# Kernel optimization log

Hardware: AMD Instinct MI355X
Metric: run time of the kernel (lower is better)

## Reference

```python
import jax, jax.numpy as jnp
import numpy as np

# ---- hyperparameters (from args defaults) ----
TEMPERATURE = 0.07
ALPHA = 0.5
OT_EPSILON = 0.1
OT_ITERS = 20
HOLO_WEIGHT = 1.0
RKD_DISTANCE_WEIGHT = 1.0
RKD_ANGLE_WEIGHT = 2.0
GLOBAL_RKD_WEIGHT = 10.0
MATRYOSHKA_DIMS = [128, 768]
MATRYOSHKA_WEIGHTS = [1.0, 2.0]

B, N, H_S, H_T, D_REP = 64, 256, 768, 1024, 768


def l2norm(x, axis=-1):
    # F.normalize(p=2): x / max(||x||, eps)
    n = jnp.sqrt(jnp.sum(x * x, axis=axis, keepdims=True))
    return x / jnp.maximum(n, 1e-12)


def pairwise_distance(x):
    # [n, d] -> [n, n] squared-euclidean-style distances
    sq = jnp.sum(x * x, axis=1, keepdims=True)
    return sq + sq.T - 2.0 * (x @ x.T)


def huber(diff):
    a = jnp.abs(diff)
    return jnp.where(a < 1.0, 0.5 * a * a, a - 0.5)


def rkd_distance_loss(s, t):
    n = s.shape[0]
    mask = jnp.triu(jnp.ones((n, n), dtype=bool), k=1)
    cnt = jnp.sum(mask.astype(s.dtype))
    ds, dt = pairwise_distance(s), pairwise_distance(t)
    mean_s = jax.lax.stop_gradient(jnp.sum(jnp.where(mask, ds, 0.0)) / cnt) + 1e-8
    mean_t = jax.lax.stop_gradient(jnp.sum(jnp.where(mask, dt, 0.0)) / cnt) + 1e-8
    loss = huber(ds / mean_s - dt / mean_t)
    return jnp.sum(jnp.where(mask, loss, 0.0)) / cnt


def angle_potentials(x):
    # diffs[i, j] = x[j] - x[i]
    diffs = x[None, :, :] - x[:, None, :]
    e = diffs / (jnp.linalg.norm(diffs, axis=-1, keepdims=True) + 1e-8)
    return jnp.einsum('ijd,kjd->ijk', e, e)


def rkd_angle_loss(s, t):
    psi_s, psi_t = angle_potentials(s), angle_potentials(t)
    n = psi_s.shape[0]
    idx = jnp.arange(n)
    i, j, k = idx[:, None, None], idx[None, :, None], idx[None, None, :]
    mask = (i != j) & (i != k) & (j != k)  # exclude degenerate triplets
    cnt = jnp.sum(mask.astype(s.dtype))
    loss = huber(psi_s - psi_t)
    return jnp.sum(jnp.where(mask, loss, 0.0)) / cnt


def saliency_measure(h, temp=1.0):
    # softmax over token axis of hidden-state norms -> [B, N, 1]
    norms = jnp.linalg.norm(h, axis=-1)
    return jax.nn.softmax(norms / temp, axis=-1)[..., None]


def structure_matrix(z):
    zn = l2norm(z, axis=-1)
    return 1.0 - jnp.einsum('bnd,bmd->bnm', zn, zn)


def sinkhorn_knopp_log_domain(C, mu, nu):
    # C: [B, Ns, Nt]; mu: [B, Ns, 1]; nu: [B, Nt, 1]
    log_K = -C / OT_EPSILON
    log_mu = jnp.log(mu + 1e-8)
    log_nu = jnp.log(nu + 1e-8)
    u = jnp.zeros_like(mu)
    v = jnp.zeros_like(nu)
    for _ in range(OT_ITERS):
        u = log_mu - jax.scipy.special.logsumexp(
            log_K + jnp.swapaxes(v, 1, 2), axis=2, keepdims=True)
        v = log_nu - jax.scipy.special.logsumexp(
            jnp.swapaxes(log_K, 1, 2) + jnp.swapaxes(u, 1, 2),
            axis=2, keepdims=True)
    return jnp.exp(u + log_K + jnp.swapaxes(v, 1, 2))


def fused_gromov_wasserstein(z_s, z_t, proj_w, proj_b):
    mu = saliency_measure(z_s)   # [B, N, 1]
    nu = saliency_measure(z_t)   # [B, N, 1]
    C_s = structure_matrix(z_s)  # [B, N, N]
    C_t = structure_matrix(z_t)
    z_s_norm = l2norm(z_s @ proj_w + proj_b, axis=-1)
    z_t_norm = l2norm(z_t, axis=-1)
    M = 1.0 - jnp.einsum('bnd,bmd->bnm', z_s_norm, z_t_norm)
    Gamma = sinkhorn_knopp_log_domain(M, mu, nu)
    feat_loss = jnp.mean(jnp.sum(M * Gamma, axis=(1, 2)))
    Gamma_norm = Gamma / (jnp.sum(Gamma, axis=2, keepdims=True) + 1e-8)
    C_t_mapped = jnp.einsum('bnm,bmk,blk->bnl', Gamma_norm, C_t, Gamma_norm)
    w = jnp.einsum('bni,bmi->bnm', mu, mu)  # mu @ mu^T
    struct_loss = jnp.mean(jnp.sum((C_s - C_t_mapped) ** 2 * w, axis=(1, 2)))
    return (1.0 - ALPHA) * feat_loss + ALPHA * struct_loss


def cross_entropy_inbatch(scores):
    # labels = arange(B)
    logZ = jax.scipy.special.logsumexp(scores, axis=1)
    return jnp.mean(logZ - jnp.diagonal(scores))


def setup_inputs() -> dict:
    key = jax.random.key(0)
    ks = jax.random.split(key, 10)
    return {
        's_q_reps': jax.random.normal(ks[0], (B, D_REP), jnp.float32),
        's_p_reps': jax.random.normal(ks[1], (B, D_REP), jnp.float32),
        't_q_reps': jax.random.normal(ks[2], (B, D_REP), jnp.float32),
        't_p_reps': jax.random.normal(ks[3], (B, D_REP), jnp.float32),
        's_q_states': jax.random.normal(ks[4], (B, N, H_S), jnp.float32),
        's_p_states': jax.random.normal(ks[5], (B, N, H_S), jnp.float32),
        't_q_states': jax.random.normal(ks[6], (B, N, H_T), jnp.float32),
        't_p_states': jax.random.normal(ks[7], (B, N, H_T), jnp.float32),
        'proj_w': jax.random.normal(ks[8], (H_S, H_T), jnp.float32) * (H_S ** -0.5),
        'proj_b': jnp.zeros((H_T,), jnp.float32),
    }


def reference(s_q_reps, s_p_reps, t_q_reps, t_p_reps,
              s_q_states, s_p_states, t_q_states, t_p_states,
              proj_w, proj_b):
    # teacher outputs are computed under torch.no_grad()
    t_q_reps = jax.lax.stop_gradient(t_q_reps)
    t_p_reps = jax.lax.stop_gradient(t_p_reps)
    t_q_states = jax.lax.stop_gradient(t_q_states)
    t_p_states = jax.lax.stop_gradient(t_p_states)

    contrastive_acc = 0.0
    holo_acc = 0.0
    rkd_acc = 0.0
    for dim, dim_weight in zip(MATRYOSHKA_DIMS, MATRYOSHKA_WEIGHTS):
        s_q_slice = l2norm(s_q_reps[:, :dim])
        s_p_slice = l2norm(s_p_reps[:, :dim])
        scores = (s_q_slice @ s_p_slice.T) / TEMPERATURE
        contrastive_acc += dim_weight * cross_entropy_inbatch(scores)
        if dim <= 128:
            s_batch = jnp.concatenate([s_q_slice, s_p_slice], axis=0)
            t_batch = jnp.concatenate(
                [l2norm(t_q_reps[:, :dim]), l2norm(t_p_reps[:, :dim])], axis=0)
            loss_dist = rkd_distance_loss(s_batch, t_batch)
            loss_angle = rkd_angle_loss(s_batch, t_batch)
            rkd_val = (RKD_DISTANCE_WEIGHT * loss_dist
                       + RKD_ANGLE_WEIGHT * loss_angle)
            rkd_acc += GLOBAL_RKD_WEIGHT * rkd_val * 2.0
        else:
            loss_q = fused_gromov_wasserstein(s_q_states, t_q_states, proj_w, proj_b)
            loss_p = fused_gromov_wasserstein(s_p_states, t_p_states, proj_w, proj_b)
            holo_acc += HOLO_WEIGHT * 0.5 * (loss_q + loss_p)
    return contrastive_acc + holo_acc + rkd_acc
```

## Files before the change

### kernel.cpp

```cpp
#include <hip/hip_runtime.h>
#include <math.h>

#define NB   64
#define NN   256
#define HSS  768
#define HTT  1024
#define ROWS (NB*NN)
#define C2LOG 14.426950408889634f

typedef unsigned short u16;
typedef __attribute__((ext_vector_type(8))) short bf16x8;
typedef __attribute__((ext_vector_type(4))) float f32x4;

#define LIDX(r,c) (((r)<<8) + (((((c)>>3) + (r)) & 31)<<3) + ((c)&7))
#define EIDX(r,c) (((r)<<7) + (((((c)>>3) + (r)) & 15)<<3) + ((c)&7))

__device__ __forceinline__ void gl16(const u16* g, u16* l){
  __builtin_amdgcn_global_load_lds(
      (const __attribute__((address_space(1))) unsigned int*)g,
      (__attribute__((address_space(3))) unsigned int*)l,
      16, 0, 0);
}

static const size_t OFF_ACC   = 0;
static const size_t OFF_SQ128 = 16;
static const size_t OFF_SP128 = OFF_SQ128 + 64*128;
static const size_t OFF_TQ128 = OFF_SP128 + 64*128;
static const size_t OFF_TP128 = OFF_TQ128 + 64*128;
static const size_t OFF_SQ768 = OFF_TP128 + 64*128;
static const size_t OFF_SP768 = OFF_SQ768 + 64*768;
static const size_t OFF_DS    = OFF_SP768 + 64*768;
static const size_t OFF_DT    = OFF_DS + 128*128;
static const size_t OFF_CS    = OFF_DT + 128*128;
static const size_t OFF_MBF   = OFF_CS  + (size_t)2*NB*NN*NN;
static const size_t OFF_ZS_BF = OFF_MBF + (size_t)NB*NN*NN;
static const size_t OFF_ZT_BF = OFF_ZS_BF + (size_t)ROWS*HSS/2;
static const size_t OFF_WT_BF = OFF_ZT_BF + (size_t)ROWS*HTT/2;
static const size_t OFF_ZSP_BF= OFF_WT_BF + (size_t)HTT*HSS/2;
static const size_t OFF_GN_BF = OFF_ZSP_BF+ (size_t)ROWS*HTT/2;
static const size_t OFF_CT_BF = OFF_GN_BF + (size_t)NB*NN*NN;
static const size_t OFF_T_BF  = OFF_ZS_BF;
static const size_t OFF_NS    = OFF_CT_BF + (size_t)NB*NN*NN;
static const size_t OFF_NT    = OFF_NS + ROWS;
static const size_t OFF_NSP   = OFF_NT + ROWS;
static const size_t OFF_MU    = OFF_NSP + ROWS;
static const size_t OFF_NU    = OFF_MU + 2*ROWS;


__device__ __forceinline__ float wred_sum(float v){
  #pragma unroll
  for(int o=32;o>0;o>>=1) v += __shfl_xor(v,o,64);
  return v;
}
__device__ __forceinline__ float wred_max(float v){
  #pragma unroll
  for(int o=32;o>0;o>>=1) v = fmaxf(v, __shfl_xor(v,o,64));
  return v;
}
__device__ __forceinline__ u16 f2bf(float f){
  unsigned u = __float_as_uint(f);
  unsigned r = (u + 0x7fffu + ((u>>16)&1u)) >> 16;
  return (u16)r;
}
__device__ __forceinline__ float bf2f(u16 h){
  return __uint_as_float(((unsigned)h)<<16);
}

__global__ __launch_bounds__(256) void k_l2norm_all(
    const float* __restrict__ sq, const float* __restrict__ sp,
    const float* __restrict__ tq, const float* __restrict__ tp,
    float* __restrict__ ws){
  int bid = blockIdx.x;
  int r = bid & 63;
  const float* in; float* out; int kuse;
  if(bid < 64)       { in = sq; out = ws + OFF_SQ128; kuse = 128; }
  else if(bid < 128) { in = sp; out = ws + OFF_SP128; kuse = 128; }
  else if(bid < 192) { in = tq; out = ws + OFF_TQ128; kuse = 128; }
  else if(bid < 256) { in = tp; out = ws + OFF_TP128; kuse = 128; }
  else if(bid < 320) { in = sq; out = ws + OFF_SQ768; kuse = 768; }
  else               { in = sp; out = ws + OFF_SP768; kuse = 768; }
  const float* row = in + (size_t)r*768;
  float ss = 0.f;
  for(int d=threadIdx.x; d<kuse; d+=256){ float x=row[d]; ss += x*x; }
  ss = wred_sum(ss);
  __shared__ float sm[4];
  if((threadIdx.x&63)==0) sm[threadIdx.x>>6]=ss;
  __syncthreads();
  float tot = sm[0]+sm[1]+sm[2]+sm[3];
  float inv = 1.f / fmaxf(sqrtf(tot), 1e-12f);
  for(int d=threadIdx.x; d<kuse; d+=256) out[(size_t)r*kuse + d] = row[d]*inv;
}

__global__ __launch_bounds__(512) void k_contrastive2(const float* __restrict__ ws,
    float* __restrict__ acc){
  int bid = blockIdx.x;
  int i = bid & 63;
  int big = bid >> 6;
  const float* q = ws + (big ? OFF_SQ768 : OFF_SQ128);
  const float* p = ws + (big ? OFF_SP768 : OFF_SP128);
  int dim = big ? 768 : 128;
  float weight = big ? 2.f : 1.f;
  int j = threadIdx.x & 63;
  int part = threadIdx.x >> 6;
  const float* qi = q + (size_t)i*dim;
  const float* pj = p + (size_t)j*dim;
  int seg = dim >> 3;
  int d0 = part*seg;
  float dot = 0.f;
  for(int d=d0; d<d0+seg; d+=4){
    float4 a = *(const float4*)(qi+d);
    float4 b = *(const float4*)(pj+d);
    dot = fmaf(a.x,b.x,dot);
    dot = fmaf(a.y,b.y,dot);
    dot = fmaf(a.z,b.z,dot);
    dot = fmaf(a.w,b.w,dot);
  }
  __shared__ float sm[8][64];
  sm[part][j] = dot;
  __syncthreads();
  if(part==0){
    float s = 0.f;
    #pragma unroll
    for(int k=0;k<8;k++) s += sm[k][j];
    s = s / 0.07f;
    float mx = wred_max(s);
    float e = expf(s - mx);
    float Z = wred_sum(e);
    float logZ = mx + logf(Z);
    float diag = __shfl(s, i, 64);
    if(j==0) atomicAdd(acc+0, weight*(logZ - diag)*(1.f/64.f));
  }
}

__global__ __launch_bounds__(128) void k_gram_ds(const float* __restrict__ sb,
    const float* __restrict__ tb, float* __restrict__ ds, float* __restrict__ dt,
    float* __restrict__ acc){
  int r = blockIdx.x, c = threadIdx.x;
  const float* sr = sb + r*128; const float* sc = sb + c*128;
  const float* tr = tb + r*128; const float* tc = tb + c*128;
  float dot_s=0,ssr=0,ssc=0,dot_t=0,tsr=0,tsc=0;
  for(int d=0; d<128; d++){
    float a=sr[d], b=sc[d]; dot_s += a*b; ssr += a*a; ssc += b*b;
    float at=tr[d], bt=tc[d]; dot_t += at*bt; tsr += at*at; tsc += bt*bt;
  }
  float dv = ssr + ssc - 2.f*dot_s;
  float tv = tsr + tsc - 2.f*dot_t;
  ds[r*128+c] = dv; dt[r*128+c] = tv;
  float ms = (c>r)? dv : 0.f;
  float mt = (c>r)? tv : 0.f;
  ms = wred_sum(ms); mt = wred_sum(mt);
  __shared__ float sm[2][2];
  if((threadIdx.x&63)==0){ sm[0][threadIdx.x>>6]=ms; sm[1][threadIdx.x>>6]=mt; }
  __syncthreads();
  if(threadIdx.x==0){ atomicAdd(acc+1, sm[0][0]+sm[0][1]); atomicAdd(acc+2, sm[1][0]+sm[1][1]); }
}

__global__ __launch_bounds__(128) void k_rkd_dist(const float* __restrict__ ds,
    const float* __restrict__ dt, float* __restrict__ acc){
  int r=blockIdx.x, c=threadIdx.x;
  float mean_s = acc[1]*(1.f/8128.f) + 1e-8f;
  float mean_t = acc[2]*(1.f/8128.f) + 1e-8f;
  float h=0.f;
  if(c>r){
    float diff = ds[r*128+c]/mean_s - dt[r*128+c]/mean_t;
    float a = fabsf(diff);
    h = (a<1.f)? 0.5f*a*a : a-0.5f;
  }
  h = wred_sum(h);
  __shared__ float sm[2];
  if((threadIdx.x&63)==0) sm[threadIdx.x>>6]=h;
  __syncthreads();
  if(threadIdx.x==0) atomicAdd(acc+3, sm[0]+sm[1]);
}

#define RKD_LDS 65536
__global__ __launch_bounds__(256, 1) void k_rkd_angle_mfma(
    const float* __restrict__ sb, const float* __restrict__ tb,
    float* __restrict__ accp)
{
  extern __shared__ u16 eSh[];
  u16* Es = eSh;
  u16* Et = eSh + 128*128;
  const int j    = blockIdx.x >> 1;
  const int half = blockIdx.x & 1;
  const int tid = threadIdx.x;
  {
    const int i = tid >> 1, h = tid & 1;
    #pragma unroll
    for(int which=0; which<2; which++){
      const float* xb = which ? tb : sb;
      u16* E = which ? Et : Es;
      const float* xj = xb + j*128 + h*64;
      const float* xi = xb + i*128 + h*64;
      float ss = 0.f;
      #pragma unroll
      for(int d4=0; d4<16; d4++){
        float4 a = *(const float4*)(xj + d4*4);
        float4 b = *(const float4*)(xi + d4*4);
        float d0=a.x-b.x, d1=a.y-b.y, d2=a.z-b.z, d3=a.w-b.w;
        ss += d0*d0+d1*d1+d2*d2+d3*d3;
      }
      ss += __shfl_xor(ss, 1, 64);
      float inv = (i==j) ? 0.f : 1.f/(sqrtf(ss)+1e-8f);
      #pragma unroll
      for(int d4=0; d4<16; d4++){
        float4 a = *(const float4*)(xj + d4*4);
        float4 b = *(const float4*)(xi + d4*4);
        int c = h*64 + d4*4;
        E[EIDX(i,c+0)] = f2bf((a.x-b.x)*inv);
        E[EIDX(i,c+1)] = f2bf((a.y-b.y)*inv);
        E[EIDX(i,c+2)] = f2bf((a.z-b.z)*inv);
        E[EIDX(i,c+3)] = f2bf((a.w-b.w)*inv);
      }
    }
  }
  __syncthreads();
  const int w = tid >> 6, lane = tid & 63;
  const int q = lane >> 4, loc = lane & 15;
  float hsum = 0.f;
  #pragma unroll
  for(int ni=0; ni<4; ni++){
    const int cb = half*64 + ni*16;
    #pragma unroll
    for(int mi=0; mi<2; mi++){
      const int rb = w*32 + mi*16;
      f32x4 as_ = {0.f,0.f,0.f,0.f}, at_ = {0.f,0.f,0.f,0.f};
      #pragma unroll
      for(int k0=0; k0<128; k0+=32){
        int ra = rb + loc, rbn = cb + loc;
        int ca = k0 + q*8;
        bf16x8 aS = *(const bf16x8*)(Es + EIDX(ra, ca));
        bf16x8 bS = *(const bf16x8*)(Es + EIDX(rbn, ca));
        bf16x8 aT = *(const bf16x8*)(Et + EIDX(ra, ca));
        bf16x8 bT = *(const bf16x8*)(Et + EIDX(rbn, ca));
        as_ = __builtin_amdgcn_mfma_f32_16x16x32_bf16(aS, bS, as_, 0,0,0);
        at_ = __builtin_amdgcn_mfma_f32_16x16x32_bf16(aT, bT, at_, 0,0,0);
      }
      #pragma unroll
      for(int jj=0; jj<4; jj++){
        int row = rb + q*4 + jj, col = cb + loc;
        if(row != col){
          float d = as_[jj] - at_[jj];
          float a = fabsf(d);
          hsum += (a < 1.f) ? 0.5f*a*a : a - 0.5f;
        }
      }
    }
  }
  hsum = wred_sum(hsum);
  __syncthreads();
  float* red = (float*)eSh;
  if(lane==0) red[w] = hsum;
  __syncthreads();
  if(tid==0) atomicAdd(accp+4, red[0]+red[1]+red[2]+red[3]);
}

__global__ __launch_bounds__(256) void k_cvt_norm(const float* __restrict__ in,
    u16* __restrict__ out, float* __restrict__ nrm, int K){
  int w = threadIdx.x >> 6, l = threadIdx.x & 63;
  int r = blockIdx.x*4 + w;
  const float* row = in + (size_t)r*K;
  u16* orow = out + (size_t)r*K;
  float ss = 0.f;
  int nv = K >> 8;
  for(int i=0;i<nv;i++){
    int d = l*4 + i*256;
    float4 x = *(const float4*)(row + d);
    ushort4 o; o.x=f2bf(x.x); o.y=f2bf(x.y); o.z=f2bf(x.z); o.w=f2bf(x.w);
    *(ushort4*)(orow + d) = o;
    ss += x.x*x.x + x.y*x.y + x.z*x.z + x.w*x.w;
  }
  ss = wred_sum(ss);
  if(l==0) nrm[r] = sqrtf(ss);
}

__global__ __launch_bounds__(256) void k_row_norm_bf16(const u16* __restrict__ z,
    float* __restrict__ nrm, int K){
  int w = threadIdx.x >> 6, l = threadIdx.x & 63;
  int r = blockIdx.x*4 + w;
  const u16* row = z + (size_t)r*K;
  float ss = 0.f;
  int nv = K >> 9;
  for(int i=0;i<nv;i++){
    int d = l*8 + i*512;
    uint4 v = *(const uint4*)(row + d);
    float a0=__uint_as_float(v.x<<16), a1=__uint_as_float(v.x&0xffff0000u);
    float a2=__uint_as_float(v.y<<16), a3=__uint_as_float(v.y&0xffff0000u);
    float a4=__uint_as_float(v.z<<16), a5=__uint_as_float(v.z&0xffff0000u);
    float a6=__uint_as_float(v.w<<16), a7=__uint_as_float(v.w&0xffff0000u);
    ss += a0*a0+a1*a1+a2*a2+a3*a3+a4*a4+a5*a5+a6*a6+a7*a7;
  }
  ss = wred_sum(ss);
  if(l==0) nrm[r] = sqrtf(ss);
}

__global__ void k_wt(const float* __restrict__ W, u16* __restrict__ Wt){
  __shared__ float t[32][33];
  int k0 = blockIdx.y*32, n0 = blockIdx.x*32;
  int tx = threadIdx.x, ty = threadIdx.y;
  for(int r=0;r<32;r+=8) t[ty+r][tx] = W[(size_t)(k0+ty+r)*HTT + n0+tx];
  __syncthreads();
  for(int r=0;r<32;r+=8) Wt[(size_t)(n0+ty+r)*HSS + k0+tx] = f2bf(t[tx][ty+r]);
}

__global__ __launch_bounds__(256) void k_saliency2(const float* __restrict__ ns,
    const float* __restrict__ nt, float* __restrict__ omu, float* __restrict__ onu){
  int b0 = blockIdx.x, n = threadIdx.x;
  const float* nrm = (b0 < NB) ? ns : nt;
  float* out = (b0 < NB) ? omu : onu;
  int b = b0 & 63;
  float x = nrm[b*NN+n];
  float mx = wred_max(x);
  __shared__ float sm[4], sm2[4];
  if((n&63)==0) sm[n>>6]=mx;
  __syncthreads();
  mx = fmaxf(fmaxf(sm[0],sm[1]),fmaxf(sm[2],sm[3]));
  float e = expf(x-mx);
  float s = wred_sum(e);
  if((n&63)==0) sm2[n>>6]=s;
  __syncthreads();
  s = sm2[0]+sm2[1]+sm2[2]+sm2[3];
  out[b*NN+n] = e/s;
}

enum { MODE_PROJ=0, MODE_COST=1, MODE_PLAIN=2, MODE_STRUCT=3 };

template<int MODE>
__global__ __launch_bounds__(256) void k_mfma(
    const u16* __restrict__ A, int lda, long bA,
    const u16* __restrict__ B, int ldb, long bB,
    int K,
    float* __restrict__ outF, u16* __restrict__ outB, int ldo, long bO,
    const float* __restrict__ nx, const float* __restrict__ ny,
    const float* __restrict__ bias,
    const float* __restrict__ Cs, const float* __restrict__ mu,
    float* __restrict__ accp)
{
  __shared__ u16 As[128*32];
  __shared__ u16 Bs[128*32];
  __shared__ float red[4];

  int gx = gridDim.x, gy = gridDim.y;
  int flat = blockIdx.x + gx*(blockIdx.y + gy*blockIdx.z);
  int nwg  = gx*gy*gridDim.z;
  int cpx  = nwg >> 3;
  int lg   = (flat & 7)*cpx + (flat >> 3);
  int bx   = lg % gx;
  int rest = lg / gx;
  int by   = rest % gy;
  int b    = rest / gy;

  const u16* Ab = A + (size_t)b*bA;
  const u16* Bb = B + (size_t)b*bB;
  int tid = threadIdx.x;
  int lane = tid & 63, w = tid >> 6;
  int m0 = by*128, n0 = bx*128;
  int row_off = (w>>1)*64, col_off = (w&1)*64;
  int q = lane>>4, loc = lane&15;
  f32x4 acc[4][4] = {};

  const int srow = (lane >> 2);
  const int sslot = lane & 3;

  for(int k0=0;k0<K;k0+=32){
    #pragma unroll
    for(int h=0;h<2;h++){
      int row = h*64 + w*16 + srow;
      int ca  = (sslot ^ ((row>>1)&3))*8;
      u16* ldst = As + h*2048 + w*512 + lane*8;
      u16* ldstB= Bs + h*2048 + w*512 + lane*8;
      gl16(Ab + (size_t)(m0+row)*lda + k0 + ca, ldst);
      gl16(Bb + (size_t)(n0+row)*ldb + k0 + ca, ldstB);
    }
    __syncthreads();
    bf16x8 af[4], bfr[4];
    #pragma unroll
    for(int mi=0;mi<4;mi++){
      int r = row_off + mi*16 + loc;
      int slot = q ^ ((r>>1)&3);
      af[mi] = *(const bf16x8*)(As + r*32 + slot*8);
    }
    #pragma unroll
    for(int ni=0;ni<4;ni++){
      int r = col_off + ni*16 + loc;
      int slot = q ^ ((r>>1)&3);
      bfr[ni] = *(const bf16x8*)(Bs + r*32 + slot*8);
    }
    #pragma unroll
    for(int mi=0;mi<4;mi++)
      #pragma unroll
      for(int ni=0;ni<4;ni++)
        acc[mi][ni] = __builtin_amdgcn_mfma_f32_16x16x32_bf16(af[mi], bfr[ni], acc[mi][ni], 0,0,0);
    __syncthreads();
  }

  float* outFb = outF ? outF + (size_t)b*bO : nullptr;
  u16*   outBb = outB ? outB + (size_t)b*bO : nullptr;
  const float* nxb = nx ? nx + (size_t)b*NN : nullptr;
  const float* nyb = ny ? ny + (size_t)b*NN : nullptr;
  const float* Cb  = (MODE==MODE_STRUCT) ? Cs + (size_t)b*bO : nullptr;
  const float* mb  = (MODE==MODE_STRUCT) ? mu + (size_t)b*NN : nullptr;
  float lsum = 0.f;
  #pragma unroll
  for(int mi=0;mi<4;mi++){
    #pragma unroll
    for(int j=0;j<4;j++){
      int row = m0 + row_off + mi*16 + q*4 + j;
      float ir = 0.f, mr = 0.f;
      if(MODE==MODE_COST)   ir = 1.f/fmaxf(nxb[row],1e-12f);
      if(MODE==MODE_STRUCT) mr = mb[row];
      #pragma unroll
      for(int ni=0;ni<4;ni++){
        int col = n0 + col_off + ni*16 + loc;
        float v = acc[mi][ni][j];
        if(MODE==MODE_PROJ){
          v += bias[col];
          outBb[(size_t)row*ldo + col] = f2bf(v);
        } else if(MODE==MODE_COST){
          float ic = 1.f/fmaxf(nyb[col],1e-12f);
          v = 1.f - v*ir*ic;
          if(outFb) outFb[(size_t)row*ldo + col] = v;
          if(outBb) outBb[(size_t)row*ldo + col] = f2bf(v);
        } else if(MODE==MODE_PLAIN){
          outBb[(size_t)row*ldo + col] = f2bf(v);
        } else {
          float d = Cb[(size_t)row*ldo + col] - v;
          lsum += d*d*mr*mb[col];
        }
      }
    }
  }
  if(MODE==MODE_STRUCT){
    lsum = wred_sum(lsum);
    if(lane==0) red[w] = lsum;
    __syncthreads();
    if(tid==0) atomicAdd(accp+6, red[0]+red[1]+red[2]+red[3]);
  }
}

#define SINK_DYN_LDS 131072
__global__ __launch_bounds__(1024, 1) void k_sinkhorn_fused(
    const u16* __restrict__ Mbf, const float* __restrict__ muL,
    const float* __restrict__ nuL, u16* __restrict__ Gn, float* __restrict__ accp)
{
  extern __shared__ u16 Ks[];
  __shared__ __align__(16) float part[4096];
  __shared__ __align__(16) float su[NN], sv[NN], smu[NN], snu[NN];
  __shared__ float red[16];

  const int b = blockIdx.x;
  const int t = threadIdx.x;
  const u16* Mb = Mbf + (size_t)b*NN*NN;

  #pragma unroll
  for(int i=0;i<16;i++){
    int e = (i*1024 + t)*4;
    int r = e>>8, c = e&255;
    ushort4 mv = *(const ushort4*)(Mb + e);
    ushort4 o;
    o.x = f2bf(exp2f(-C2LOG*bf2f(mv.x)));
    o.y = f2bf(exp2f(-C2LOG*bf2f(mv.y)));
    o.z = f2bf(exp2f(-C2LOG*bf2f(mv.z)));
    o.w = f2bf(exp2f(-C2LOG*bf2f(mv.w)));
    *(ushort4*)(Ks + LIDX(r,c)) = o;
  }
  if(t < NN){
    smu[t] = muL[(size_t)b*NN+t] + 1e-8f;
    snu[t] = nuL[(size_t)b*NN+t] + 1e-8f;
    sv[t] = 1.f;
  }
  __syncthreads();

  const int r_ = t & 255, p_ = t >> 8;
  const int w = t>>6, l = t&63;

  for(int it=0; it<20; it++){
    {
      float s0=0.f, s1=0.f, s2=0.f, s3=0.f;
      #pragma unroll
      for(int jj=0;jj<8;jj++){
        int c0 = p_*64 + jj*8;
        uint4 kv = *(const uint4*)(Ks + LIDX(r_, c0));
        float4 va = *(const float4*)(sv + c0);
        float4 vb = *(const float4*)(sv + c0 + 4);
        s0 = fmaf(__uint_as_float(kv.x<<16),           va.x, s0);
        s1 = fmaf(__uint_as_float(kv.x & 0xffff0000u), va.y, s1);
        s2 = fmaf(__uint_as_float(kv.y<<16),           va.z, s2);
        s3 = fmaf(__uint_as_float(kv.y & 0xffff0000u), va.w, s3);
        s0 = fmaf(__uint_as_float(kv.z<<16),           vb.x, s0);
        s1 = fmaf(__uint_as_float(kv.z & 0xffff0000u), vb.y, s1);
        s2 = fmaf(__uint_as_float(kv.w<<16),           vb.z, s2);
        s3 = fmaf(__uint_as_float(kv.w & 0xffff0000u), vb.w, s3);
      }
      part[t] = (s0+s1)+(s2+s3);
    }
    __syncthreads();
    if(t < NN){
      float S = part[t] + part[256+t] + part[512+t] + part[768+t];
      su[t] = smu[t] / S;
    }
    __syncthreads();
    {
      float cs0=0.f,cs1=0.f,cs2=0.f,cs3=0.f;
      #pragma unroll
      for(int rr=0;rr<16;rr++){
        int r = w*16 + rr;
        ushort4 kv = *(const ushort4*)(Ks + LIDX(r, l*4));
        float ur = su[r];
        cs0 = fmaf(bf2f(kv.x), ur, cs0);
        cs1 = fmaf(bf2f(kv.y), ur, cs1);
        cs2 = fmaf(bf2f(kv.z), ur, cs2);
        cs3 = fmaf(bf2f(kv.w), ur, cs3);
      }
      float4 o; o.x=cs0; o.y=cs1; o.z=cs2; o.w=cs3;
      *(float4*)(part + w*256 + l*4) = o;
    }
    __syncthreads();
    if(t < NN){
      float S = 0.f;
      #pragma unroll
      for(int ww=0;ww<16;ww++) S += part[ww*256 + t];
      sv[t] = snu[t] / S;
    }
    __syncthreads();
  }

  {
    float s0=0.f, s1=0.f, s2=0.f, s3=0.f;
    #pragma unroll
    for(int jj=0;jj<8;jj++){
      int c0 = p_*64 + jj*8;
      uint4 kv = *(const uint4*)(Ks + LIDX(r_, c0));
      float4 va = *(const float4*)(sv + c0);
      float4 vb = *(const float4*)(sv + c0 + 4);
      s0 = fmaf(__uint_as_float(kv.x<<16),           va.x, s0);
      s1 = fmaf(__uint_as_float(kv.x & 0xffff0000u), va.y, s1);
      s2 = fmaf(__uint_as_float(kv.y<<16),           va.z, s2);
      s3 = fmaf(__uint_as_float(kv.y & 0xffff0000u), va.w, s3);
      s0 = fmaf(__uint_as_float(kv.z<<16),           vb.x, s0);
      s1 = fmaf(__uint_as_float(kv.z & 0xffff0000u), vb.y, s1);
      s2 = fmaf(__uint_as_float(kv.w<<16),           vb.z, s2);
      s3 = fmaf(__uint_as_float(kv.w & 0xffff0000u), vb.w, s3);
    }
    part[t] = (s0+s1)+(s2+s3);
  }
  __syncthreads();
  if(t < NN){
    float S = part[t] + part[256+t] + part[512+t] + part[768+t];
    smu[t] = 1.f / (su[t]*S + 1e-8f);
  }
  __syncthreads();

  u16* Gb = Gn + (size_t)b*NN*NN;
  const float IC = -1.f/C2LOG;
  float v0 = sv[l*4+0], v1 = sv[l*4+1], v2 = sv[l*4+2], v3 = sv[l*4+3];
  float fl = 0.f;
  for(int rr=0;rr<16;rr++){
    int r = w*16 + rr;
    ushort4 kv = *(const ushort4*)(Ks + LIDX(r, l*4));
    float k0=bf2f(kv.x), k1=bf2f(kv.y), k2=bf2f(kv.z), k3=bf2f(kv.w);
    float ur = su[r], inv = smu[r];
    float g0=ur*k0*v0, g1=ur*k1*v1, g2=ur*k2*v2, g3=ur*k3*v3;
    fl += g0*(__log2f(k0)*IC) + g1*(__log2f(k1)*IC)
        + g2*(__log2f(k2)*IC) + g3*(__log2f(k3)*IC);
    ushort4 o;
    o.x=f2bf(g0*inv); o.y=f2bf(g1*inv); o.z=f2bf(g2*inv); o.w=f2bf(g3*inv);
    *(ushort4*)(Gb + (size_t)r*NN + l*4) = o;
  }
  fl = wred_sum(fl);
  if(l==0) red[w] = fl;
  __syncthreads();
  if(t==0){
    float s=0.f;
    #pragma unroll
    for(int i=0;i<16;i++) s+=red[i];
    atomicAdd(accp+5, s);
  }
}

__global__ void k_final(const float* __restrict__ acc, float* __restrict__ out){
  out[0] = acc[0]
         + 20.f*acc[3]*(1.f/8128.f)
         + 40.f*acc[4]*(1.f/2048256.f)
         + 0.25f*(acc[5]+acc[6])*(1.f/64.f);
}

extern "C" void kernel_launch(void* const* d_in, const int* in_sizes, int n_in,
                              void* d_out, int out_size, void* d_ws, size_t ws_size,
                              hipStream_t stream) {
  const float* s_q_reps   = (const float*)d_in[0];
  const float* s_p_reps   = (const float*)d_in[1];
  const float* t_q_reps   = (const float*)d_in[2];
  const float* t_p_reps   = (const float*)d_in[3];
  const float* s_q_states = (const float*)d_in[4];
  const float* s_p_states = (const float*)d_in[5];
  const float* t_q_states = (const float*)d_in[6];
  const float* t_p_states = (const float*)d_in[7];
  const float* proj_w     = (const float*)d_in[8];
  const float* proj_b     = (const float*)d_in[9];
  float* ws = (float*)d_ws;
  float* acc = ws + OFF_ACC;
  u16* M_BF   = (u16*)(ws + OFF_MBF);
  u16* ZS_BF  = (u16*)(ws + OFF_ZS_BF);
  u16* ZT_BF  = (u16*)(ws + OFF_ZT_BF);
  u16* WT_BF  = (u16*)(ws + OFF_WT_BF);
  u16* ZSP_BF = (u16*)(ws + OFF_ZSP_BF);
  u16* GN_BF  = (u16*)(ws + OFF_GN_BF);
  u16* CT_BF  = (u16*)(ws + OFF_CT_BF);
  u16* T_BF   = (u16*)(ws + OFF_T_BF);

  hipFuncSetAttribute(reinterpret_cast<const void*>(k_sinkhorn_fused),
                      hipFuncAttributeMaxDynamicSharedMemorySize, SINK_DYN_LDS);
  hipFuncSetAttribute(reinterpret_cast<const void*>(k_rkd_angle_mfma),
                      hipFuncAttributeMaxDynamicSharedMemorySize, RKD_LDS);

  hipMemsetAsync(acc, 0, 16*sizeof(float), stream);

  k_l2norm_all<<<384,256,0,stream>>>(s_q_reps, s_p_reps, t_q_reps, t_p_reps, ws);
  k_contrastive2<<<128,512,0,stream>>>(ws, acc);
  k_gram_ds<<<128,128,0,stream>>>(ws+OFF_SQ128, ws+OFF_TQ128, ws+OFF_DS, ws+OFF_DT, acc);
  k_rkd_dist<<<128,128,0,stream>>>(ws+OFF_DS, ws+OFF_DT, acc);
  k_rkd_angle_mfma<<<256,256,RKD_LDS,stream>>>(ws+OFF_SQ128, ws+OFF_TQ128, acc);

  k_wt<<<dim3(HTT/32, HSS/32),dim3(32,8),0,stream>>>(proj_w, WT_BF);

  for(int pass=0; pass<2; pass++){
    const float* zs = pass ? s_p_states : s_q_states;
    const float* zt = pass ? t_p_states : t_q_states;
    size_t po  = (size_t)pass*NB*NN*NN;
    size_t pr  = (size_t)pass*ROWS;
    k_cvt_norm<<<ROWS/4,256,0,stream>>>(zs, ZS_BF, ws+OFF_NS, HSS);
    k_cvt_norm<<<ROWS/4,256,0,stream>>>(zt, ZT_BF, ws+OFF_NT, HTT);
    k_saliency2<<<128,256,0,stream>>>(ws+OFF_NS, ws+OFF_NT, ws+OFF_MU+pr, ws+OFF_NU+pr);
    k_mfma<MODE_PROJ><<<dim3(HTT/128, ROWS/128, 1),256,0,stream>>>(
        ZS_BF, HSS, 0, WT_BF, HSS, 0, HSS,
        nullptr, ZSP_BF, HTT, 0,
        nullptr, nullptr, proj_b, nullptr, nullptr, nullptr);
    k_row_norm_bf16<<<ROWS/4,256,0,stream>>>(ZSP_BF, ws+OFF_NSP, HTT);
    k_mfma<MODE_COST><<<dim3(2,2,NB),256,0,stream>>>(
        ZS_BF, HSS, (long)NN*HSS, ZS_BF, HSS, (long)NN*HSS, HSS,
        ws+OFF_CS+po, nullptr, NN, (long)NN*NN,
        ws+OFF_NS, ws+OFF_NS, nullptr, nullptr, nullptr, nullptr);
    k_mfma<MODE_COST><<<dim3(2,2,NB),256,0,stream>>>(
        ZT_BF, HTT, (long)NN*HTT, ZT_BF, HTT, (long)NN*HTT, HTT,
        nullptr, CT_BF+po, NN, (long)NN*NN,
        ws+OFF_NT, ws+OFF_NT, nullptr, nullptr, nullptr, nullptr);
    k_mfma<MODE_COST><<<dim3(2,2,NB),256,0,stream>>>(
        ZSP_BF, HTT, (long)NN*HTT, ZT_BF, HTT, (long)NN*HTT, HTT,
        nullptr, M_BF+po, NN, (long)NN*NN,
        ws+OFF_NSP, ws+OFF_NT, nullptr, nullptr, nullptr, nullptr);
  }

  k_sinkhorn_fused<<<2*NB,1024,SINK_DYN_LDS,stream>>>(
      M_BF, ws+OFF_MU, ws+OFF_NU, GN_BF, acc);

  k_mfma<MODE_PLAIN><<<dim3(2,2,2*NB),256,0,stream>>>(
      GN_BF, NN, (long)NN*NN, CT_BF, NN, (long)NN*NN, NN,
      nullptr, T_BF, NN, (long)NN*NN,
      nullptr, nullptr, nullptr, nullptr, nullptr, nullptr);
  k_mfma<MODE_STRUCT><<<dim3(2,2,2*NB),256,0,stream>>>(
      T_BF, NN, (long)NN*NN, GN_BF, NN, (long)NN*NN, NN,
      nullptr, nullptr, NN, (long)NN*NN,
      nullptr, nullptr, nullptr, ws+OFF_CS, ws+OFF_MU, acc);

  k_final<<<1,1,0,stream>>>(acc, (float*)d_out);
}
```

Baseline: 671.5 us.

## Merge small prep kernels and use 64x64 MFMA tiles for batched cost GEMMs

Fuses the bf16 conversion and norm kernels for both state tensors with the RKD gram computation into one launch, and merges the RKD distance reduction with the pass-0 saliency softmax into another. Adds a 64x64-tile MFMA GEMM variant with XCD-aware block remapping and uses it for the per-batch 256x256 cost, plain and structure GEMMs. This raises block count from 256 to 1024+ per launch to fill more CUs. The trade-off is less reuse per tile and a single-buffered K loop with two barriers per step.

```diff
diff --git a/kernel.cpp b/kernel.cpp
--- a/kernel.cpp
+++ b/kernel.cpp
@@ -132,45 +132,106 @@
   }
 }
 
-__global__ __launch_bounds__(128) void k_gram_ds(const float* __restrict__ sb,
-    const float* __restrict__ tb, float* __restrict__ ds, float* __restrict__ dt,
-    float* __restrict__ acc){
-  int r = blockIdx.x, c = threadIdx.x;
-  const float* sr = sb + r*128; const float* sc = sb + c*128;
-  const float* tr = tb + r*128; const float* tc = tb + c*128;
-  float dot_s=0,ssr=0,ssc=0,dot_t=0,tsr=0,tsc=0;
-  for(int d=0; d<128; d++){
-    float a=sr[d], b=sc[d]; dot_s += a*b; ssr += a*a; ssc += b*b;
-    float at=tr[d], bt=tc[d]; dot_t += at*bt; tsr += at*at; tsc += bt*bt;
-  }
-  float dv = ssr + ssc - 2.f*dot_s;
-  float tv = tsr + tsc - 2.f*dot_t;
-  ds[r*128+c] = dv; dt[r*128+c] = tv;
-  float ms = (c>r)? dv : 0.f;
-  float mt = (c>r)? tv : 0.f;
-  ms = wred_sum(ms); mt = wred_sum(mt);
+__global__ __launch_bounds__(256) void k_pack_cvt(
+    const float* __restrict__ zs, const float* __restrict__ zt,
+    u16* __restrict__ zsb, u16* __restrict__ ztb,
+    float* __restrict__ ns, float* __restrict__ nt,
+    const float* __restrict__ sb128, const float* __restrict__ tb128,
+    float* __restrict__ ds, float* __restrict__ dt, float* __restrict__ acc)
+{
   __shared__ float sm[2][2];
-  if((threadIdx.x&63)==0){ sm[0][threadIdx.x>>6]=ms; sm[1][threadIdx.x>>6]=mt; }
-  __syncthreads();
-  if(threadIdx.x==0){ atomicAdd(acc+1, sm[0][0]+sm[0][1]); atomicAdd(acc+2, sm[1][0]+sm[1][1]); }
-}
-
-__global__ __launch_bounds__(128) void k_rkd_dist(const float* __restrict__ ds,
-    const float* __restrict__ dt, float* __restrict__ acc){
-  int r=blockIdx.x, c=threadIdx.x;
-  float mean_s = acc[1]*(1.f/8128.f) + 1e-8f;
-  float mean_t = acc[2]*(1.f/8128.f) + 1e-8f;
-  float h=0.f;
-  if(c>r){
-    float diff = ds[r*128+c]/mean_s - dt[r*128+c]/mean_t;
-    float a = fabsf(diff);
-    h = (a<1.f)? 0.5f*a*a : a-0.5f;
-  }
-  h = wred_sum(h);
-  __shared__ float sm[2];
-  if((threadIdx.x&63)==0) sm[threadIdx.x>>6]=h;
-  __syncthreads();
-  if(threadIdx.x==0) atomicAdd(acc+3, sm[0]+sm[1]);
+  int bid = blockIdx.x;
+  if(bid < 8192){
+    const float* in; u16* out; float* nrm; int K; int cb;
+    if(bid < 4096){ in=zs; out=zsb; nrm=ns; K=HSS; cb=bid; }
+    else          { in=zt; out=ztb; nrm=nt; K=HTT; cb=bid-4096; }
+    int w = threadIdx.x >> 6, l = threadIdx.x & 63;
+    int r = cb*4 + w;
+    const float* row = in + (size_t)r*K;
+    u16* orow = out + (size_t)r*K;
+    float ss = 0.f;
+    int nv = K >> 8;
+    for(int i=0;i<nv;i++){
+      int d = l*4 + i*256;
+      float4 x = *(const float4*)(row + d);
+      ushort4 o; o.x=f2bf(x.x); o.y=f2bf(x.y); o.z=f2bf(x.z); o.w=f2bf(x.w);
+      *(ushort4*)(orow + d) = o;
+      ss += x.x*x.x + x.y*x.y + x.z*x.z + x.w*x.w;
+    }
+    ss = wred_sum(ss);
+    if(l==0) nrm[r] = sqrtf(ss);
+    return;
+  }
+  {
+    int r = bid - 8192;
+    int c = threadIdx.x;
+    float ms = 0.f, mt = 0.f;
+    if(c < 128){
+      const float* sr = sb128 + r*128; const float* sc = sb128 + c*128;
+      const float* tr = tb128 + r*128; const float* tc = tb128 + c*128;
+      float dot_s=0,ssr=0,ssc=0,dot_t=0,tsr=0,tsc=0;
+      for(int d=0; d<128; d++){
+        float a=sr[d], bb=sc[d]; dot_s += a*bb; ssr += a*a; ssc += bb*bb;
+        float at=tr[d], bt=tc[d]; dot_t += at*bt; tsr += at*at; tsc += bt*bt;
+      }
+      float dv = ssr + ssc - 2.f*dot_s;
+      float tv = tsr + tsc - 2.f*dot_t;
+      ds[r*128+c] = dv; dt[r*128+c] = tv;
+      ms = (c>r)? dv : 0.f;
+      mt = (c>r)? tv : 0.f;
+      ms = wred_sum(ms); mt = wred_sum(mt);
+      if((c&63)==0){ sm[0][c>>6]=ms; sm[1][c>>6]=mt; }
+    }
+    __syncthreads();
+    if(threadIdx.x==0){
+      atomicAdd(acc+1, sm[0][0]+sm[0][1]);
+      atomicAdd(acc+2, sm[1][0]+sm[1][1]);
+    }
+  }
+}
+
+__global__ __launch_bounds__(256) void k_small0(
+    const float* __restrict__ ds, const float* __restrict__ dt,
+    const float* __restrict__ ns, const float* __restrict__ nt,
+    float* __restrict__ omu, float* __restrict__ onu, float* __restrict__ acc)
+{
+  __shared__ float sm[4], sm2[4];
+  int bid = blockIdx.x;
+  if(bid < 128){
+    int r = bid, c = threadIdx.x;
+    float mean_s = acc[1]*(1.f/8128.f) + 1e-8f;
+    float mean_t = acc[2]*(1.f/8128.f) + 1e-8f;
+    float h = 0.f;
+    if(c < 128){
+      if(c > r){
+        float diff = ds[r*128+c]/mean_s - dt[r*128+c]/mean_t;
+        float a = fabsf(diff);
+        h = (a<1.f)? 0.5f*a*a : a-0.5f;
+      }
+      h = wred_sum(h);
+      if((c&63)==0) sm[c>>6]=h;
+    }
+    __syncthreads();
+    if(threadIdx.x==0) atomicAdd(acc+3, sm[0]+sm[1]);
+    return;
+  }
+  {
+    int b0 = bid - 128, n = threadIdx.x;
+    const float* nrm = (b0 < NB) ? ns : nt;
+    float* out = (b0 < NB) ? omu : onu;
+    int b = b0 & 63;
+    float x = nrm[b*NN+n];
+    float mx = wred_max(x);
+    if((n&63)==0) sm[n>>6]=mx;
+    __syncthreads();
+    mx = fmaxf(fmaxf(sm[0],sm[1]),fmaxf(sm[2],sm[3]));
+    float e = expf(x-mx);
+    float s = wred_sum(e);
+    if((n&63)==0) sm2[n>>6]=s;
+    __syncthreads();
+    s = sm2[0]+sm2[1]+sm2[2]+sm2[3];
+    out[b*NN+n] = e/s;
+  }
 }
 
 #define RKD_LDS 65536
@@ -253,25 +314,6 @@
   if(lane==0) red[w] = hsum;
   __syncthreads();
   if(tid==0) atomicAdd(accp+4, red[0]+red[1]+red[2]+red[3]);
-}
-
-__global__ __launch_bounds__(256) void k_cvt_norm(const float* __restrict__ in,
-    u16* __restrict__ out, float* __restrict__ nrm, int K){
-  int w = threadIdx.x >> 6, l = threadIdx.x & 63;
-  int r = blockIdx.x*4 + w;
-  const float* row = in + (size_t)r*K;
-  u16* orow = out + (size_t)r*K;
-  float ss = 0.f;
-  int nv = K >> 8;
-  for(int i=0;i<nv;i++){
-    int d = l*4 + i*256;
-    float4 x = *(const float4*)(row + d);
-    ushort4 o; o.x=f2bf(x.x); o.y=f2bf(x.y); o.z=f2bf(x.z); o.w=f2bf(x.w);
-    *(ushort4*)(orow + d) = o;
-    ss += x.x*x.x + x.y*x.y + x.z*x.z + x.w*x.w;
-  }
-  ss = wred_sum(ss);
-  if(l==0) nrm[r] = sqrtf(ss);
 }
 
 __global__ __launch_bounds__(256) void k_row_norm_bf16(const u16* __restrict__ z,
@@ -411,6 +453,118 @@
       if(MODE==MODE_STRUCT) mr = mb[row];
       #pragma unroll
       for(int ni=0;ni<4;ni++){
+        int col = n0 + col_off + ni*16 + loc;
+        float v = acc[mi][ni][j];
+        if(MODE==MODE_PROJ){
+          v += bias[col];
+          outBb[(size_t)row*ldo + col] = f2bf(v);
+        } else if(MODE==MODE_COST){
+          float ic = 1.f/fmaxf(nyb[col],1e-12f);
+          v = 1.f - v*ir*ic;
+          if(outFb) outFb[(size_t)row*ldo + col] = v;
+          if(outBb) outBb[(size_t)row*ldo + col] = f2bf(v);
+        } else if(MODE==MODE_PLAIN){
+          outBb[(size_t)row*ldo + col] = f2bf(v);
+        } else {
+          float d = Cb[(size_t)row*ldo + col] - v;
+          lsum += d*d*mr*mb[col];
+        }
+      }
+    }
+  }
+  if(MODE==MODE_STRUCT){
+    lsum = wred_sum(lsum);
+    if(lane==0) red[w] = lsum;
+    __syncthreads();
+    if(tid==0) atomicAdd(accp+6, red[0]+red[1]+red[2]+red[3]);
+  }
+}
+
+template<int MODE>
+__global__ __launch_bounds__(256) void k_mfma64(
+    const u16* __restrict__ A, int lda, long bA,
+    const u16* __restrict__ B, int ldb, long bB,
+    int K,
+    float* __restrict__ outF, u16* __restrict__ outB, int ldo, long bO,
+    const float* __restrict__ nx, const float* __restrict__ ny,
+    const float* __restrict__ bias,
+    const float* __restrict__ Cs, const float* __restrict__ mu,
+    float* __restrict__ accp)
+{
+  __shared__ u16 As[64*32];
+  __shared__ u16 Bs[64*32];
+  __shared__ float red[4];
+
+  int gx = gridDim.x, gy = gridDim.y;
+  int flat = blockIdx.x + gx*(blockIdx.y + gy*blockIdx.z);
+  int nwg  = gx*gy*gridDim.z;
+  int cpx  = nwg >> 3;
+  int lg   = (flat & 7)*cpx + (flat >> 3);
+  int bx   = lg % gx;
+  int rest = lg / gx;
+  int by   = rest % gy;
+  int b    = rest / gy;
+
+  const u16* Ab = A + (size_t)b*bA;
+  const u16* Bb = B + (size_t)b*bB;
+  int tid = threadIdx.x;
+  int lane = tid & 63, w = tid >> 6;
+  int m0 = by*64, n0 = bx*64;
+  int row_off = (w>>1)*32, col_off = (w&1)*32;
+  int q = lane>>4, loc = lane&15;
+  f32x4 acc[2][2] = {};
+
+  const int srow = tid >> 2;
+  const int sslot = tid & 3;
+
+  for(int k0=0;k0<K;k0+=32){
+    {
+      int row = srow;
+      int ca  = (sslot ^ ((row>>1)&3))*8;
+      u16* la = As + w*512 + lane*8;
+      u16* lb = Bs + w*512 + lane*8;
+      gl16(Ab + (size_t)(m0+row)*lda + k0 + ca, la);
+      gl16(Bb + (size_t)(n0+row)*ldb + k0 + ca, lb);
+    }
+    __syncthreads();
+    bf16x8 af[2], bfr[2];
+    #pragma unroll
+    for(int mi=0;mi<2;mi++){
+      int r = row_off + mi*16 + loc;
+      int slot = q ^ ((r>>1)&3);
+      af[mi] = *(const bf16x8*)(As + r*32 + slot*8);
+    }
+    #pragma unroll
+    for(int ni=0;ni<2;ni++){
+      int r = col_off + ni*16 + loc;
+      int slot = q ^ ((r>>1)&3);
+      bfr[ni] = *(const bf16x8*)(Bs + r*32 + slot*8);
+    }
+    #pragma unroll
+    for(int mi=0;mi<2;mi++)
+      #pragma unroll
+      for(int ni=0;ni<2;ni++)
+        acc[mi][ni] = __builtin_amdgcn_mfma_f32_16x16x32_bf16(af[mi], bfr[ni], acc[mi][ni], 0,0,0);
+    __syncthreads();
+  }
+
+  float* outFb = outF ? outF + (size_t)b*bO : nullptr;
+  u16*   outBb = outB ? outB + (size_t)b*bO : nullptr;
+  const float* nxb = nx ? nx + (size_t)b*NN : nullptr;
+  const float* nyb = ny ? ny + (size_t)b*NN : nullptr;
+  const float* Cb  = (MODE==MODE_STRUCT) ? Cs + (size_t)b*bO : nullptr;
+  const float* mb  = (MODE==MODE_STRUCT) ? mu + (size_t)b*NN : nullptr;
+  float lsum = 0.f;
+  #pragma unroll
+  for(int mi=0;mi<2;mi++){
+    #pragma unroll
+    for(int j=0;j<4;j++){
+      int row = m0 + row_off + mi*16 + q*4 + j;
+      float ir = 0.f, mr = 0.f;
+      if(MODE==MODE_COST)   ir = 1.f/fmaxf(nxb[row],1e-12f);
+      if(MODE==MODE_STRUCT) mr = mb[row];
+      #pragma unroll
+      for(int ni=0;ni<2;ni++){
         int col = n0 + col_off + ni*16 + loc;
         float v = acc[mi][ni][j];
         if(MODE==MODE_PROJ){
@@ -618,34 +772,36 @@
 
   k_l2norm_all<<<384,256,0,stream>>>(s_q_reps, s_p_reps, t_q_reps, t_p_reps, ws);
   k_contrastive2<<<128,512,0,stream>>>(ws, acc);
-  k_gram_ds<<<128,128,0,stream>>>(ws+OFF_SQ128, ws+OFF_TQ128, ws+OFF_DS, ws+OFF_DT, acc);
-  k_rkd_dist<<<128,128,0,stream>>>(ws+OFF_DS, ws+OFF_DT, acc);
+
+  k_pack_cvt<<<8320,256,0,stream>>>(s_q_states, t_q_states, ZS_BF, ZT_BF,
+      ws+OFF_NS, ws+OFF_NT, ws+OFF_SQ128, ws+OFF_TQ128, ws+OFF_DS, ws+OFF_DT, acc);
+  k_small0<<<256,256,0,stream>>>(ws+OFF_DS, ws+OFF_DT, ws+OFF_NS, ws+OFF_NT,
+      ws+OFF_MU, ws+OFF_NU, acc);
   k_rkd_angle_mfma<<<256,256,RKD_LDS,stream>>>(ws+OFF_SQ128, ws+OFF_TQ128, acc);
-
   k_wt<<<dim3(HTT/32, HSS/32),dim3(32,8),0,stream>>>(proj_w, WT_BF);
 
   for(int pass=0; pass<2; pass++){
-    const float* zs = pass ? s_p_states : s_q_states;
-    const float* zt = pass ? t_p_states : t_q_states;
     size_t po  = (size_t)pass*NB*NN*NN;
     size_t pr  = (size_t)pass*ROWS;
-    k_cvt_norm<<<ROWS/4,256,0,stream>>>(zs, ZS_BF, ws+OFF_NS, HSS);
-    k_cvt_norm<<<ROWS/4,256,0,stream>>>(zt, ZT_BF, ws+OFF_NT, HTT);
-    k_saliency2<<<128,256,0,stream>>>(ws+OFF_NS, ws+OFF_NT, ws+OFF_MU+pr, ws+OFF_NU+pr);
+    if(pass==1){
+      k_pack_cvt<<<8192,256,0,stream>>>(s_p_states, t_p_states, ZS_BF, ZT_BF,
+          ws+OFF_NS, ws+OFF_NT, ws+OFF_SQ128, ws+OFF_TQ128, ws+OFF_DS, ws+OFF_DT, acc);
+      k_saliency2<<<128,256,0,stream>>>(ws+OFF_NS, ws+OFF_NT, ws+OFF_MU+pr, ws+OFF_NU+pr);
+    }
     k_mfma<MODE_PROJ><<<dim3(HTT/128, ROWS/128, 1),256,0,stream>>>(
         ZS_BF, HSS, 0, WT_BF, HSS, 0, HSS,
         nullptr, ZSP_BF, HTT, 0,
         nullptr, nullptr, proj_b, nullptr, nullptr, nullptr);
     k_row_norm_bf16<<<ROWS/4,256,0,stream>>>(ZSP_BF, ws+OFF_NSP, HTT);
-    k_mfma<MODE_COST><<<dim3(2,2,NB),256,0,stream>>>(
+    k_mfma64<MODE_COST><<<dim3(4,4,NB),256,0,stream>>>(
         ZS_BF, HSS, (long)NN*HSS, ZS_BF, HSS, (long)NN*HSS, HSS,
         ws+OFF_CS+po, nullptr, NN, (long)NN*NN,
         ws+OFF_NS, ws+OFF_NS, nullptr, nullptr, nullptr, nullptr);
-    k_mfma<MODE_COST><<<dim3(2,2,NB),256,0,stream>>>(
+    k_mfma64<MODE_COST><<<dim3(4,4,NB),256,0,stream>>>(
         ZT_BF, HTT, (long)NN*HTT, ZT_BF, HTT, (long)NN*HTT, HTT,
         nullptr, CT_BF+po, NN, (long)NN*NN,
         ws+OFF_NT, ws+OFF_NT, nullptr, nullptr, nullptr, nullptr);
-    k_mfma<MODE_COST><<<dim3(2,2,NB),256,0,stream>>>(
+    k_mfma64<MODE_COST><<<dim3(4,4,NB),256,0,stream>>>(
         ZSP_BF, HTT, (long)NN*HTT, ZT_BF, HTT, (long)NN*HTT, HTT,
         nullptr, M_BF+po, NN, (long)NN*NN,
         ws+OFF_NSP, ws+OFF_NT, nullptr, nullptr, nullptr, nullptr);
@@ -654,11 +810,11 @@
   k_sinkhorn_fused<<<2*NB,1024,SINK_DYN_LDS,stream>>>(
       M_BF, ws+OFF_MU, ws+OFF_NU, GN_BF, acc);
 
-  k_mfma<MODE_PLAIN><<<dim3(2,2,2*NB),256,0,stream>>>(
+  k_mfma64<MODE_PLAIN><<<dim3(4,4,2*NB),256,0,stream>>>(
       GN_BF, NN, (long)NN*NN, CT_BF, NN, (long)NN*NN, NN,
       nullptr, T_BF, NN, (long)NN*NN,
       nullptr, nullptr, nullptr, nullptr, nullptr, nullptr);
-  k_mfma<MODE_STRUCT><<<dim3(2,2,2*NB),256,0,stream>>>(
+  k_mfma64<MODE_STRUCT><<<dim3(4,4,2*NB),256,0,stream>>>(
       T_BF, NN, (long)NN*NN, GN_BF, NN, (long)NN*NN, NN,
       nullptr, nullptr, NN, (long)NN*NN,
       nullptr, nullptr, nullptr, ws+OFF_CS, ws+OFF_MU, acc);
```

New measurement: 634.6 us. 1.06x faster.
